# Kernel optimization log

Hardware: AMD Instinct MI355X
Metric: run time of the kernel (lower is better)

## Reference

```python
import jax, jax.numpy as jnp
import numpy as np

K_INTERACT = 8  # k nearest context nodes per target hyperedge


def setup_inputs() -> dict:
    key = jax.random.key(0)
    ks = jax.random.split(key, 7)
    B, C, H, W = 4, 256, 64, 64
    s = 1.0 / np.sqrt(C).astype(np.float32)
    return {
        "X_target": jax.random.normal(ks[0], (B, C, H, W), jnp.float32),
        "X_context1": jax.random.normal(ks[1], (B, C, H, W), jnp.float32),
        "X_context2": jax.random.normal(ks[2], (B, C, H, W), jnp.float32),
        # HypergraphConv params: node2edge Linear (W1,b1), edge2node Linear (W2,b2)
        "W1": jax.random.normal(ks[3], (C, C), jnp.float32) * s,
        "b1": jax.random.normal(ks[4], (C,), jnp.float32) * s,
        "W2": jax.random.normal(ks[5], (C, C), jnp.float32) * s,
        "b2": jax.random.normal(ks[6], (C,), jnp.float32) * s,
    }


def _hypergraph_one(Xt, Xc, W1, b1, W2, b2, k):
    """Per-batch hypergraph message passing, sparse form of H^T X / H X.
    Xt: [N, C] target nodes, Xc: [Nc, C] context nodes.
    Edge j = {target j} U {k nearest context nodes of target j}.
    Equivalent to dense H_i [N+Nc, N] with degree normalization.
    """
    N, C = Xt.shape
    Nc = Xc.shape[0]
    # squared Euclidean cdist (same argmins as torch.cdist), knn = smallest-k
    d2 = (jnp.sum(Xt * Xt, axis=1)[:, None]
          + jnp.sum(Xc * Xc, axis=1)[None, :]
          - 2.0 * (Xt @ Xc.T))                      # [N, Nc]
    _, knn = jax.lax.top_k(-d2, k)                   # [N, k] context indices

    # node2edge linear transform on all nodes
    Xn_t = Xt @ W1 + b1                              # [N, C]
    Xn_c = Xc @ W1 + b1                              # [Nc, C]

    # X_edge = (H^T @ Xn) / deg_e ; deg_e = k+1 (self + k distinct knn)
    gathered = Xn_c[knn]                             # [N, k, C]
    X_edge = (Xn_t + gathered.sum(axis=1)) / jnp.float32(k + 1)

    # edge2node linear transform
    X_et = X_edge @ W2 + b2                          # [N, C]

    # X_node_new = (H @ X_et) / deg_v
    # target node v belongs only to edge v -> deg_v = 1
    out_t = X_et
    # context node c sums X_et[j] over edges j that selected it
    flat = knn.reshape(-1)                           # [N*k]
    contrib = jax.ops.segment_sum(
        jnp.broadcast_to(X_et[:, None, :], (N, k, C)).reshape(N * k, C),
        flat, num_segments=Nc)                       # [Nc, C]
    counts = jax.ops.segment_sum(jnp.ones((N * k,), jnp.float32),
                                 flat, num_segments=Nc)
    out_c = contrib / jnp.clip(counts, 1.0)[:, None]  # deg_v clamp_min(1)
    return out_t, out_c


def reference(X_target, X_context1, X_context2, W1, b1, W2, b2):
    B, C, H, W = X_target.shape
    N = H * W
    to_nodes = lambda x: x.transpose(0, 2, 3, 1).reshape(B, N, C)
    Xt = to_nodes(X_target)                                       # [B, N, C]
    Xc = jnp.concatenate([to_nodes(X_context1), to_nodes(X_context2)],
                         axis=1)                                  # [B, 2N, C]
    f = lambda xt, xc: _hypergraph_one(xt, xc, W1, b1, W2, b2, K_INTERACT)
    out_t, out_c = jax.vmap(f)(Xt, Xc)
    to_img = lambda x: x.reshape(B, H, W, C).transpose(0, 3, 1, 2)
    return (to_img(out_t), to_img(out_c[:, :N]), to_img(out_c[:, N:]))
```

## Files before the change

### kernel.cpp

```cpp
#include <hip/hip_runtime.h>
#include <math.h>
#include <float.h>

#define BATCH 4
#define CH    256
#define NT    4096
#define NCTX  8192
#define KI    8

#define CSEL    10
#define DNSPLIT 8
#define CTX_PER (NCTX / DNSPLIT)
#define NTILE   (CTX_PER / 32)
#define NKEY    (DNSPLIT * CSEL)
#define RESC    12

typedef __attribute__((ext_vector_type(8)))  __bf16 bf16x8;
typedef __attribute__((ext_vector_type(16))) float  f32x16;

__device__ __forceinline__ unsigned short bf16_rne(float v) {
  unsigned u = __float_as_uint(v);
  return (unsigned short)((u + 0x7fffu + ((u >> 16) & 1u)) >> 16);
}

__global__ __launch_bounds__(256) void k_transpose2(const float* __restrict__ Xt,
                                                    const float* __restrict__ Xc1,
                                                    const float* __restrict__ Xc2,
                                                    float* __restrict__ Q,
                                                    float* __restrict__ P,
                                                    unsigned short* __restrict__ XtBh,
                                                    unsigned short* __restrict__ XtBl,
                                                    unsigned short* __restrict__ XcBh,
                                                    unsigned short* __restrict__ XcBl,
                                                    float* __restrict__ nrm) {
  __shared__ float tile[64][33];
  __shared__ float ps[8][32];
  const int which = blockIdx.z >> 2, b = blockIdx.z & 3;
  const float* src;
  float* dF; unsigned short *dH, *dL; float* nrmp = nullptr;
  if (which == 0) {
    src = Xt + (long)b * CH * NT;
    dF = Q + (long)b * NT * CH;
    dH = XtBh + (long)b * NT * CH;  dL = XtBl + (long)b * NT * CH;
  } else if (which == 1) {
    src = Xc1 + (long)b * CH * NT;
    dF = P + (long)b * NCTX * CH;
    dH = XcBh + (long)b * NCTX * CH;  dL = XcBl + (long)b * NCTX * CH;
    nrmp = nrm + (long)b * NCTX;
  } else {
    src = Xc2 + (long)b * CH * NT;
    dF = P + ((long)b * NCTX + NT) * CH;
    dH = XcBh + ((long)b * NCTX + NT) * CH;  dL = XcBl + ((long)b * NCTX + NT) * CH;
    nrmp = nrm + (long)b * NCTX + NT;
  }
  const int m0 = blockIdx.x * 32, c0 = blockIdx.y * 64;
  const int tx = threadIdx.x, ty = threadIdx.y;
  float part = 0.f;
#pragma unroll
  for (int i = ty; i < 64; i += 8) {
    float v = src[(long)(c0 + i) * NT + (m0 + tx)];
    tile[i][tx] = v;
    part = fmaf(v, v, part);
  }
  if (which) ps[ty][tx] = part;
  __syncthreads();
#pragma unroll
  for (int i = ty; i < 32; i += 8) {
    float v0 = tile[2 * tx][i];
    float v1 = tile[2 * tx + 1][i];
    long o = (long)(m0 + i) * CH + (c0 + 2 * tx);
    float2 f2; f2.x = v0; f2.y = v1;
    *(float2*)&dF[o] = f2;
    unsigned short h0 = bf16_rne(v0), h1 = bf16_rne(v1);
    ushort2 h2; h2.x = h0; h2.y = h1;
    *(ushort2*)&dH[o] = h2;
    float hf0 = __uint_as_float((unsigned)h0 << 16);
    float hf1 = __uint_as_float((unsigned)h1 << 16);
    ushort2 l2; l2.x = bf16_rne(v0 - hf0); l2.y = bf16_rne(v1 - hf1);
    *(ushort2*)&dL[o] = l2;
  }
  if (which && ty == 0) {
    float s = 0.f;
#pragma unroll
    for (int j = 0; j < 8; ++j) s += ps[j][tx];
    atomicAdd(&nrmp[m0 + tx], -0.5f * s);
  }
}

__global__ __launch_bounds__(256) void k_wtrans(const float* __restrict__ W1,
                                                const float* __restrict__ W2,
                                                unsigned short* __restrict__ WT1h,
                                                unsigned short* __restrict__ WT1l,
                                                unsigned short* __restrict__ WT2h,
                                                unsigned short* __restrict__ WT2l) {
  __shared__ float tile[32][33];
  const float* W = blockIdx.z ? W2 : W1;
  unsigned short* WTh = blockIdx.z ? WT2h : WT1h;
  unsigned short* WTl = blockIdx.z ? WT2l : WT1l;
  const int n0 = blockIdx.x * 32, k0 = blockIdx.y * 32;
  const int tx = threadIdx.x, ty = threadIdx.y;
#pragma unroll
  for (int i = ty; i < 32; i += 8)
    tile[i][tx] = W[(k0 + i) * CH + (n0 + tx)];
  __syncthreads();
#pragma unroll
  for (int i = ty; i < 32; i += 8) {
    float v = tile[tx][i];
    int o = (n0 + i) * CH + (k0 + tx);
    unsigned short h = bf16_rne(v);
    WTh[o] = h;
    float hf = __uint_as_float((unsigned)h << 16);
    WTl[o] = bf16_rne(v - hf);
  }
}

__global__ __launch_bounds__(256) void k_dist_mfma(const __bf16* __restrict__ XcB,
                                                   const __bf16* __restrict__ XtB,
                                                   const float* __restrict__ nrm,
                                                   unsigned* __restrict__ cand) {
  __shared__ __bf16 lds[2][32 * CH];
  const int b = blockIdx.y, split = blockIdx.z;
  const int t = threadIdx.x, w = t >> 6, lane = t & 63;
  const int l31 = lane & 31, lh = lane >> 5;
  const int tgt0 = blockIdx.x * 128 + w * 32;
  const int cbase = split * CTX_PER;
  const float* nrmt = nrm + (long)b * NCTX + cbase;

  const __bf16* tp = XtB + ((long)b * NT + tgt0 + l31) * CH + lh * 8;
  bf16x8 bfrag[16];
#pragma unroll
  for (int s = 0; s < 16; ++s) bfrag[s] = *(const bf16x8*)(tp + s * 16);

  unsigned kd[CSEL];
#pragma unroll
  for (int q = 0; q < CSEL; ++q) kd[q] = 0xFFFFFFFFu;

  const __bf16* cp = XcB + ((long)b * NCTX + cbase + l31) * CH;

  auto STAGE = [&](int buf, int jt) {
#pragma unroll
    for (int r = 0; r < 4; ++r) {
      int c = r * 4 + w;
      const __bf16* src = cp + (long)jt * 32 * CH + (c * 2 + lh) * 8;
      __bf16* dst = &lds[buf][c * 512];
      __builtin_amdgcn_global_load_lds((const __attribute__((address_space(1))) void*)src,
                                       (__attribute__((address_space(3))) void*)dst,
                                       16, 0, 0);
    }
  };

  STAGE(0, 0);
  __syncthreads();

  int cur = 0;
  for (int jt = 0; jt < NTILE; ++jt) {
    if (jt + 1 < NTILE) STAGE(cur ^ 1, jt + 1);

    const int ct0 = jt * 32;
    f32x16 acc;
#pragma unroll
    for (int g = 0; g < 4; ++g) {
      float4 nv = *(const float4*)&nrmt[ct0 + 8 * g + 4 * lh];
      acc[4 * g + 0] = nv.x; acc[4 * g + 1] = nv.y;
      acc[4 * g + 2] = nv.z; acc[4 * g + 3] = nv.w;
    }
#pragma unroll
    for (int s = 0; s < 16; ++s) {
      bf16x8 a = *(const bf16x8*)(&lds[cur][s * 512 + lane * 8]);
      acc = __builtin_amdgcn_mfma_f32_32x32x16_bf16(a, bfrag[s], acc, 0, 0, 0);
    }

#pragma unroll
    for (int reg = 0; reg < 16; ++reg) {
      const int row = (reg & 3) + 8 * (reg >> 2) + lh * 4;
      float sc = fmaf(acc[reg], -2.0f, 512.0f);
      unsigned key = (__float_as_uint(sc) & 0xFFFFF800u) | (unsigned)ct0 | (unsigned)row;
#pragma unroll
      for (int q = 0; q < CSEL; ++q) {
        unsigned lo = min(key, kd[q]);
        key = max(key, kd[q]);
        kd[q] = lo;
      }
    }
    __syncthreads();
    cur ^= 1;
  }

  unsigned oth[CSEL];
#pragma unroll
  for (int q = 0; q < CSEL; ++q) oth[q] = (unsigned)__shfl_xor((int)kd[q], 32, 64);
  if (lh == 0) {
    long ob = (((long)b * NT + tgt0 + l31) * DNSPLIT + split) * CSEL;
#pragma unroll
    for (int q = 0; q < CSEL; ++q)
      cand[ob + q] = min(kd[q], oth[CSEL - 1 - q]);
  }
}

__global__ __launch_bounds__(64) void k_rescore(const float* __restrict__ XtT,
                                                const float* __restrict__ XcT,
                                                const unsigned* __restrict__ cand,
                                                int* __restrict__ knn,
                                                unsigned* __restrict__ counts) {
  const int n = blockIdx.x, b = blockIdx.y, lane = threadIdx.x;
  const int grp = lane >> 4, gl = lane & 15;
  __shared__ unsigned sk[NKEY];
  __shared__ int cidx[RESC];
  __shared__ double sd[RESC];
  __shared__ int sj[RESC];
  const unsigned* kp = cand + ((long)b * NT + n) * NKEY;
  unsigned k0 = kp[lane];
  unsigned k1 = (lane < NKEY - 64) ? kp[64 + lane] : 0xFFFFFFFFu;
  sk[lane] = k0;
  if (lane < NKEY - 64) sk[64 + lane] = k1;
  __syncthreads();
  int r0 = 0, r1 = 0;
  for (int i = 0; i < NKEY; ++i) {
    unsigned s = sk[i];
    r0 += (s < k0 || (s == k0 && i < lane)) ? 1 : 0;
    r1 += (s < k1 || (s == k1 && i < 64 + lane)) ? 1 : 0;
  }
  if (r0 < RESC) cidx[r0] = (lane / CSEL) * CTX_PER + (int)(k0 & 0x7FFu);
  if (lane < NKEY - 64 && r1 < RESC)
    cidx[r1] = ((64 + lane) / CSEL) * CTX_PER + (int)(k1 & 0x7FFu);
  __syncthreads();

  const float* xt = XtT + ((long)b * NT + n) * CH + gl * 16;
  double xa[16];
#pragma unroll
  for (int r = 0; r < 4; ++r) {
    float4 v = *(const float4*)(xt + r * 4);
    xa[4 * r + 0] = (double)v.x; xa[4 * r + 1] = (double)v.y;
    xa[4 * r + 2] = (double)v.z; xa[4 * r + 3] = (double)v.w;
  }
#pragma unroll
  for (int q0 = 0; q0 < RESC; q0 += 4) {
    int q = q0 + grp;
    int j = cidx[q];
    const float* xc = XcT + ((long)b * NCTX + j) * CH + gl * 16;
    double acc = 0.0;
#pragma unroll
    for (int r = 0; r < 4; ++r) {
      float4 v = *(const float4*)(xc + r * 4);
      double d0 = xa[4 * r + 0] - (double)v.x; acc = fma(d0, d0, acc);
      double d1 = xa[4 * r + 1] - (double)v.y; acc = fma(d1, d1, acc);
      double d2 = xa[4 * r + 2] - (double)v.z; acc = fma(d2, d2, acc);
      double d3 = xa[4 * r + 3] - (double)v.w; acc = fma(d3, d3, acc);
    }
#pragma unroll
    for (int off = 8; off > 0; off >>= 1) acc += __shfl_xor(acc, off, 64);
    if (gl == 0) { sd[q] = acc; sj[q] = j; }
  }
  __syncthreads();
  double dq = (lane < RESC) ? sd[lane] : DBL_MAX;
  int    jq = (lane < RESC) ? sj[lane] : 0x7fffffff;
  int rank = 0;
#pragma unroll
  for (int i = 0; i < RESC; ++i) {
    double di = sd[i]; int ji = sj[i];
    rank += (di < dq || (di == dq && ji < jq)) ? 1 : 0;
  }
  if (lane < RESC && rank < KI) {
    knn[((long)b * NT + n) * KI + rank] = jq;
    atomicAdd(&counts[(long)b * NCTX + jq], 1u);
  }
}

__global__ __launch_bounds__(256) void k_gemm_mfma(const unsigned short* __restrict__ Ah,
                                                   const unsigned short* __restrict__ Al,
                                                   const unsigned short* __restrict__ WTh,
                                                   const unsigned short* __restrict__ WTl,
                                                   const float* __restrict__ bias,
                                                   float* __restrict__ out, int M) {
  __shared__ __bf16 ldsH[32 * CH];
  __shared__ __bf16 ldsL[32 * CH];
  const int b = blockIdx.y;
  const int m0 = blockIdx.x * 32;
  const int t = threadIdx.x, w = t >> 6, lane = t & 63;
  const int l31 = lane & 31, lh = lane >> 5;
  const long abase = (long)b * M * CH;
  const unsigned short* pH = Ah + abase + (long)(m0 + l31) * CH;
  const unsigned short* pL = Al + abase + (long)(m0 + l31) * CH;
#pragma unroll
  for (int r = 0; r < 4; ++r) {
    int c = r * 4 + w;
    __builtin_amdgcn_global_load_lds(
        (const __attribute__((address_space(1))) void*)(pH + (c * 2 + lh) * 8),
        (__attribute__((address_space(3))) void*)&ldsH[c * 512], 16, 0, 0);
    __builtin_amdgcn_global_load_lds(
        (const __attribute__((address_space(1))) void*)(pL + (c * 2 + lh) * 8),
        (__attribute__((address_space(3))) void*)&ldsL[c * 512], 16, 0, 0);
  }
  __syncthreads();

  const int n0 = w * 64;
  f32x16 acc0, acc1;
#pragma unroll
  for (int i = 0; i < 16; ++i) { acc0[i] = 0.f; acc1[i] = 0.f; }
#pragma unroll
  for (int s = 0; s < 16; ++s) {
    bf16x8 ah = *(const bf16x8*)&ldsH[s * 512 + lane * 8];
    bf16x8 al = *(const bf16x8*)&ldsL[s * 512 + lane * 8];
    const int koff = lh * 8 + s * 16;
    bf16x8 bh0 = *(const bf16x8*)&WTh[(n0 + l31) * CH + koff];
    bf16x8 bl0 = *(const bf16x8*)&WTl[(n0 + l31) * CH + koff];
    bf16x8 bh1 = *(const bf16x8*)&WTh[(n0 + 32 + l31) * CH + koff];
    bf16x8 bl1 = *(const bf16x8*)&WTl[(n0 + 32 + l31) * CH + koff];
    acc0 = __builtin_amdgcn_mfma_f32_32x32x16_bf16(ah, bh0, acc0, 0, 0, 0);
    acc1 = __builtin_amdgcn_mfma_f32_32x32x16_bf16(ah, bh1, acc1, 0, 0, 0);
    acc0 = __builtin_amdgcn_mfma_f32_32x32x16_bf16(ah, bl0, acc0, 0, 0, 0);
    acc1 = __builtin_amdgcn_mfma_f32_32x32x16_bf16(ah, bl1, acc1, 0, 0, 0);
    acc0 = __builtin_amdgcn_mfma_f32_32x32x16_bf16(al, bh0, acc0, 0, 0, 0);
    acc1 = __builtin_amdgcn_mfma_f32_32x32x16_bf16(al, bh1, acc1, 0, 0, 0);
  }
  float* ob = out + abase;
  float bi0 = bias[n0 + l31], bi1 = bias[n0 + 32 + l31];
#pragma unroll
  for (int reg = 0; reg < 16; ++reg) {
    int row = (reg & 3) + 8 * (reg >> 2) + 4 * lh;
    ob[(long)(m0 + row) * CH + n0 + l31]      = acc0[reg] + bi0;
    ob[(long)(m0 + row) * CH + n0 + 32 + l31] = acc1[reg] + bi1;
  }
}

__global__ __launch_bounds__(256) void k_gather(const float* __restrict__ Xn_t,
                                                const float* __restrict__ Xn_c,
                                                const int* __restrict__ knn,
                                                unsigned short* __restrict__ XeH,
                                                unsigned short* __restrict__ XeL) {
  const int n = blockIdx.x, b = blockIdx.y, c = threadIdx.x;
  const int* kn = knn + ((long)b * NT + n) * KI;
  int j[KI];
#pragma unroll
  for (int q = 0; q < KI; ++q) j[q] = kn[q];
  float acc = Xn_t[((long)b * NT + n) * CH + c];
#pragma unroll
  for (int q = 0; q < KI; ++q) acc += Xn_c[((long)b * NCTX + j[q]) * CH + c];
  float xe = acc / 9.0f;
  long o = ((long)b * NT + n) * CH + c;
  unsigned short h = bf16_rne(xe);
  XeH[o] = h;
  float hf = __uint_as_float((unsigned)h << 16);
  XeL[o] = bf16_rne(xe - hf);
}

__global__ __launch_bounds__(256) void k_scatter(const float* __restrict__ Xet,
                                                 const int* __restrict__ knn,
                                                 float* __restrict__ contrib) {
  const int n = blockIdx.x, b = blockIdx.y, c = threadIdx.x;
  const float v = Xet[((long)b * NT + n) * CH + c];
  const int* kn = knn + ((long)b * NT + n) * KI;
#pragma unroll
  for (int q = 0; q < KI; ++q)
    atomicAdd(&contrib[((long)b * NCTX + kn[q]) * CH + c], v);
}

__global__ __launch_bounds__(256) void k_fin_t(const float* __restrict__ Xet,
                                               float* __restrict__ out) {
  __shared__ float tile[32][33];
  const int b = blockIdx.z;
  const int n0 = blockIdx.x * 32, c0 = blockIdx.y * 32;
  const int tx = threadIdx.x, ty = threadIdx.y;
#pragma unroll
  for (int i = ty; i < 32; i += 8)
    tile[i][tx] = Xet[((long)b * NT + n0 + i) * CH + c0 + tx];
  __syncthreads();
#pragma unroll
  for (int i = ty; i < 32; i += 8)
    out[((long)b * CH + c0 + i) * NT + n0 + tx] = tile[tx][i];
}

__global__ __launch_bounds__(256) void k_fin_c(const float* __restrict__ contrib,
                                               const unsigned* __restrict__ counts,
                                               float* __restrict__ out1,
                                               float* __restrict__ out2) {
  __shared__ float tile[32][33];
  const int b = blockIdx.z;
  const int j0 = blockIdx.x * 32, c0 = blockIdx.y * 32;
  const int tx = threadIdx.x, ty = threadIdx.y;
#pragma unroll
  for (int i = ty; i < 32; i += 8) {
    float cnt = fmaxf((float)counts[(long)b * NCTX + j0 + i], 1.0f);
    tile[i][tx] = contrib[((long)b * NCTX + j0 + i) * CH + c0 + tx] / cnt;
  }
  __syncthreads();
  float* outp = (j0 < NT) ? (out1 + (long)b * CH * NT + j0)
                          : (out2 + (long)b * CH * NT + (j0 - NT));
#pragma unroll
  for (int i = ty; i < 32; i += 8)
    outp[(long)(c0 + i) * NT + tx] = tile[tx][i];
}

extern "C" void kernel_launch(void* const* d_in, const int* in_sizes, int n_in,
                              void* d_out, int out_size, void* d_ws, size_t ws_size,
                              hipStream_t stream) {
  const float* Xt  = (const float*)d_in[0];
  const float* Xc1 = (const float*)d_in[1];
  const float* Xc2 = (const float*)d_in[2];
  const float* W1  = (const float*)d_in[3];
  const float* b1  = (const float*)d_in[4];
  const float* W2  = (const float*)d_in[5];
  const float* b2  = (const float*)d_in[6];
  float* out = (float*)d_out;

  float* P = (float*)d_ws;
  float* Q = P + (long)BATCH * NCTX * CH;
  float* R = Q + (long)BATCH * NT * CH;
  float* nrm = R + (long)BATCH * NT * CH;
  unsigned* counts = (unsigned*)(nrm + (long)BATCH * NCTX);
  int* knn = (int*)(counts + (long)BATCH * NCTX);
  unsigned short* WT1h = (unsigned short*)(knn + (long)BATCH * NT * KI);
  unsigned short* WT1l = WT1h + CH * CH;
  unsigned short* WT2h = WT1l + CH * CH;
  unsigned short* WT2l = WT2h + CH * CH;

  unsigned* cand = (unsigned*)R;

  unsigned short* XcBh = (unsigned short*)d_out;
  unsigned short* XtBh = XcBh + (long)BATCH * NCTX * CH;
  unsigned short* XcBl = XtBh + (long)BATCH * NT * CH;
  unsigned short* XtBl = XcBl + (long)BATCH * NCTX * CH;

  float* Xn_c = P;
  float* Xn_t = R;
  unsigned short* XeH = (unsigned short*)Q;
  unsigned short* XeL = XeH + (long)BATCH * NT * CH;

  float* out_t  = out;
  float* out_c1 = out + (long)BATCH * CH * NT;
  float* out_c2 = out + 2L * BATCH * CH * NT;

  dim3 tb(32, 8);

  hipMemsetAsync(nrm, 0, (size_t)BATCH * NCTX * 8, stream);

  k_wtrans<<<dim3(8, 8, 2), tb, 0, stream>>>(W1, W2, WT1h, WT1l, WT2h, WT2l);

  k_transpose2<<<dim3(NT / 32, CH / 64, 12), tb, 0, stream>>>(
      Xt, Xc1, Xc2, Q, P, XtBh, XtBl, XcBh, XcBl, nrm);

  k_dist_mfma<<<dim3(NT / 128, BATCH, DNSPLIT), 256, 0, stream>>>(
      (const __bf16*)XcBh, (const __bf16*)XtBh, nrm, cand);

  k_rescore<<<dim3(NT, BATCH), 64, 0, stream>>>(Q, P, cand, knn, counts);

  k_gemm_mfma<<<dim3(NT / 32, BATCH), 256, 0, stream>>>(XtBh, XtBl, WT1h, WT1l, b1, Xn_t, NT);
  k_gemm_mfma<<<dim3(NCTX / 32, BATCH), 256, 0, stream>>>(XcBh, XcBl, WT1h, WT1l, b1, Xn_c, NCTX);

  k_gather<<<dim3(NT, BATCH), 256, 0, stream>>>(Xn_t, Xn_c, knn, XeH, XeL);

  k_gemm_mfma<<<dim3(NT / 32, BATCH), 256, 0, stream>>>(XeH, XeL, WT2h, WT2l, b2, R, NT);

  k_fin_t<<<dim3(NT / 32, CH / 32, BATCH), tb, 0, stream>>>(R, out_t);

  hipMemsetAsync(P, 0, (size_t)BATCH * NCTX * CH * 4, stream);
  k_scatter<<<dim3(NT, BATCH), 256, 0, stream>>>(R, knn, P);
  k_fin_c<<<dim3(NCTX / 32, CH / 32, BATCH), tb, 0, stream>>>(P, counts, out_c1, out_c2);
}
```

Baseline: 437.2 us.

## Fuse gather, edge2node GEMM and target transpose; skip top-k inserts; remap dist grid

```diff
diff --git a/kernel.cpp b/kernel.cpp
--- a/kernel.cpp
+++ b/kernel.cpp
@@ -119,10 +119,13 @@
                                                    const float* __restrict__ nrm,
                                                    unsigned* __restrict__ cand) {
   __shared__ __bf16 lds[2][32 * CH];
-  const int b = blockIdx.y, split = blockIdx.z;
+  const int lid = blockIdx.x;
+  const int xk = lid & 7, rest = lid >> 3;
+  const int b = xk >> 1, jh = xk & 1;
+  const int jw = rest & 15, split = rest >> 4;
   const int t = threadIdx.x, w = t >> 6, lane = t & 63;
   const int l31 = lane & 31, lh = lane >> 5;
-  const int tgt0 = blockIdx.x * 128 + w * 32;
+  const int tgt0 = (jh * 16 + jw) * 128 + w * 32;
   const int cbase = split * CTX_PER;
   const float* nrmt = nrm + (long)b * NCTX + cbase;
 
@@ -175,11 +178,13 @@
       const int row = (reg & 3) + 8 * (reg >> 2) + lh * 4;
       float sc = fmaf(acc[reg], -2.0f, 512.0f);
       unsigned key = (__float_as_uint(sc) & 0xFFFFF800u) | (unsigned)ct0 | (unsigned)row;
-#pragma unroll
-      for (int q = 0; q < CSEL; ++q) {
-        unsigned lo = min(key, kd[q]);
-        key = max(key, kd[q]);
-        kd[q] = lo;
+      if (__any(key < kd[CSEL - 1])) {
+#pragma unroll
+        for (int q = 0; q < CSEL; ++q) {
+          unsigned lo = min(key, kd[q]);
+          key = max(key, kd[q]);
+          kd[q] = lo;
+        }
       }
     }
     __syncthreads();
@@ -323,25 +328,116 @@
   }
 }
 
-__global__ __launch_bounds__(256) void k_gather(const float* __restrict__ Xn_t,
-                                                const float* __restrict__ Xn_c,
-                                                const int* __restrict__ knn,
-                                                unsigned short* __restrict__ XeH,
-                                                unsigned short* __restrict__ XeL) {
-  const int n = blockIdx.x, b = blockIdx.y, c = threadIdx.x;
-  const int* kn = knn + ((long)b * NT + n) * KI;
-  int j[KI];
-#pragma unroll
-  for (int q = 0; q < KI; ++q) j[q] = kn[q];
-  float acc = Xn_t[((long)b * NT + n) * CH + c];
-#pragma unroll
-  for (int q = 0; q < KI; ++q) acc += Xn_c[((long)b * NCTX + j[q]) * CH + c];
-  float xe = acc / 9.0f;
-  long o = ((long)b * NT + n) * CH + c;
-  unsigned short h = bf16_rne(xe);
-  XeH[o] = h;
-  float hf = __uint_as_float((unsigned)h << 16);
-  XeL[o] = bf16_rne(xe - hf);
+__global__ __launch_bounds__(256) void k_gg2(const float* __restrict__ Xn_c,
+                                             const int* __restrict__ knn,
+                                             const unsigned short* __restrict__ WTh,
+                                             const unsigned short* __restrict__ WTl,
+                                             const float* __restrict__ bias,
+                                             float* __restrict__ out_t,
+                                             float* __restrict__ R) {
+  __shared__ char smem[34816];
+  int* knn_s = (int*)smem;
+  __bf16* XeH = (__bf16*)(smem + 1024);
+  __bf16* XeL = (__bf16*)(smem + 17408);
+  const int b = blockIdx.y;
+  const int m0 = blockIdx.x * 32;
+  const int t = threadIdx.x, w = t >> 6, lane = t & 63;
+  const int l31 = lane & 31, lh = lane >> 5;
+
+  knn_s[t] = knn[((long)b * NT + m0 + (t >> 3)) * KI + (t & 7)];
+  __syncthreads();
+
+  const int n = t & 31, cg = t >> 5;
+  int idx[KI];
+#pragma unroll
+  for (int q = 0; q < KI; ++q) idx[q] = knn_s[n * KI + q];
+  const float* trow = R + ((long)b * NT + m0 + n) * CH;
+  const float* cb = Xn_c + (long)b * NCTX * CH;
+#pragma unroll
+  for (int kk = 0; kk < 4; ++kk) {
+    const int c = cg * 32 + kk * 8;
+    float xe[8];
+    float4 a0 = *(const float4*)(trow + c);
+    float4 a1 = *(const float4*)(trow + c + 4);
+    xe[0]=a0.x; xe[1]=a0.y; xe[2]=a0.z; xe[3]=a0.w;
+    xe[4]=a1.x; xe[5]=a1.y; xe[6]=a1.z; xe[7]=a1.w;
+#pragma unroll
+    for (int q = 0; q < KI; ++q) {
+      const float* crow = cb + (long)idx[q] * CH + c;
+      float4 c0 = *(const float4*)(crow);
+      float4 c1 = *(const float4*)(crow + 4);
+      xe[0]+=c0.x; xe[1]+=c0.y; xe[2]+=c0.z; xe[3]+=c0.w;
+      xe[4]+=c1.x; xe[5]+=c1.y; xe[6]+=c1.z; xe[7]+=c1.w;
+    }
+    unsigned h8[8], l8[8];
+#pragma unroll
+    for (int e = 0; e < 8; ++e) {
+      float v = xe[e] / 9.0f;
+      unsigned short h = bf16_rne(v);
+      h8[e] = h;
+      float hf = __uint_as_float((unsigned)h << 16);
+      l8[e] = bf16_rne(v - hf);
+    }
+    const int k8 = cg * 4 + kk;
+    const int off = (k8 >> 1) * 512 + ((k8 & 1) * 32 + n) * 8;
+    uint4 ph, pl;
+    ph.x = h8[0] | (h8[1] << 16); ph.y = h8[2] | (h8[3] << 16);
+    ph.z = h8[4] | (h8[5] << 16); ph.w = h8[6] | (h8[7] << 16);
+    pl.x = l8[0] | (l8[1] << 16); pl.y = l8[2] | (l8[3] << 16);
+    pl.z = l8[4] | (l8[5] << 16); pl.w = l8[6] | (l8[7] << 16);
+    *(uint4*)(XeH + off) = ph;
+    *(uint4*)(XeL + off) = pl;
+  }
+  __syncthreads();
+
+  const unsigned short* wh0 = WTh + (long)(w * 64 + l31) * CH;
+  const unsigned short* wl0 = WTl + (long)(w * 64 + l31) * CH;
+  f32x16 acc0, acc1;
+#pragma unroll
+  for (int i = 0; i < 16; ++i) { acc0[i] = 0.f; acc1[i] = 0.f; }
+#pragma unroll
+  for (int s = 0; s < 16; ++s) {
+    const int koff = lh * 8 + s * 16;
+    bf16x8 beh = *(const bf16x8*)&XeH[s * 512 + lane * 8];
+    bf16x8 bel = *(const bf16x8*)&XeL[s * 512 + lane * 8];
+    bf16x8 ah0 = *(const bf16x8*)(const __bf16*)(wh0 + koff);
+    bf16x8 al0 = *(const bf16x8*)(const __bf16*)(wl0 + koff);
+    bf16x8 ah1 = *(const bf16x8*)(const __bf16*)(wh0 + 32 * CH + koff);
+    bf16x8 al1 = *(const bf16x8*)(const __bf16*)(wl0 + 32 * CH + koff);
+    acc0 = __builtin_amdgcn_mfma_f32_32x32x16_bf16(ah0, beh, acc0, 0, 0, 0);
+    acc1 = __builtin_amdgcn_mfma_f32_32x32x16_bf16(ah1, beh, acc1, 0, 0, 0);
+    acc0 = __builtin_amdgcn_mfma_f32_32x32x16_bf16(al0, beh, acc0, 0, 0, 0);
+    acc1 = __builtin_amdgcn_mfma_f32_32x32x16_bf16(al1, beh, acc1, 0, 0, 0);
+    acc0 = __builtin_amdgcn_mfma_f32_32x32x16_bf16(ah0, bel, acc0, 0, 0, 0);
+    acc1 = __builtin_amdgcn_mfma_f32_32x32x16_bf16(ah1, bel, acc1, 0, 0, 0);
+  }
+  __syncthreads();
+
+  float* S = (float*)smem;
+  float* ot = out_t + (long)b * CH * NT + m0;
+#pragma unroll
+  for (int reg = 0; reg < 16; ++reg) {
+    const int row = (reg & 3) + 8 * (reg >> 2) + 4 * lh;
+    const int ch0 = w * 64 + row, ch1 = ch0 + 32;
+    float v0 = acc0[reg] + bias[ch0];
+    float v1 = acc1[reg] + bias[ch1];
+    S[ch0 * 33 + l31] = v0;
+    S[ch1 * 33 + l31] = v1;
+    ot[(long)ch0 * NT + l31] = v0;
+    ot[(long)ch1 * NT + l31] = v1;
+  }
+  __syncthreads();
+  float* rrow = R + ((long)b * NT + m0 + n) * CH;
+#pragma unroll
+  for (int kk = 0; kk < 8; ++kk) {
+    const int c = cg * 32 + kk * 4;
+    float4 v;
+    v.x = S[(c + 0) * 33 + n];
+    v.y = S[(c + 1) * 33 + n];
+    v.z = S[(c + 2) * 33 + n];
+    v.w = S[(c + 3) * 33 + n];
+    *(float4*)(rrow + c) = v;
+  }
 }
 
 __global__ __launch_bounds__(256) void k_scatter(const float* __restrict__ Xet,
@@ -353,21 +449,6 @@
 #pragma unroll
   for (int q = 0; q < KI; ++q)
     atomicAdd(&contrib[((long)b * NCTX + kn[q]) * CH + c], v);
-}
-
-__global__ __launch_bounds__(256) void k_fin_t(const float* __restrict__ Xet,
-                                               float* __restrict__ out) {
-  __shared__ float tile[32][33];
-  const int b = blockIdx.z;
-  const int n0 = blockIdx.x * 32, c0 = blockIdx.y * 32;
-  const int tx = threadIdx.x, ty = threadIdx.y;
-#pragma unroll
-  for (int i = ty; i < 32; i += 8)
-    tile[i][tx] = Xet[((long)b * NT + n0 + i) * CH + c0 + tx];
-  __syncthreads();
-#pragma unroll
-  for (int i = ty; i < 32; i += 8)
-    out[((long)b * CH + c0 + i) * NT + n0 + tx] = tile[tx][i];
 }
 
 __global__ __launch_bounds__(256) void k_fin_c(const float* __restrict__ contrib,
@@ -423,8 +504,6 @@
 
   float* Xn_c = P;
   float* Xn_t = R;
-  unsigned short* XeH = (unsigned short*)Q;
-  unsigned short* XeL = XeH + (long)BATCH * NT * CH;
 
   float* out_t  = out;
   float* out_c1 = out + (long)BATCH * CH * NT;
@@ -439,7 +518,7 @@
   k_transpose2<<<dim3(NT / 32, CH / 64, 12), tb, 0, stream>>>(
       Xt, Xc1, Xc2, Q, P, XtBh, XtBl, XcBh, XcBl, nrm);
 
-  k_dist_mfma<<<dim3(NT / 128, BATCH, DNSPLIT), 256, 0, stream>>>(
+  k_dist_mfma<<<dim3(1024), 256, 0, stream>>>(
       (const __bf16*)XcBh, (const __bf16*)XtBh, nrm, cand);
 
   k_rescore<<<dim3(NT, BATCH), 64, 0, stream>>>(Q, P, cand, knn, counts);
@@ -447,11 +526,7 @@
   k_gemm_mfma<<<dim3(NT / 32, BATCH), 256, 0, stream>>>(XtBh, XtBl, WT1h, WT1l, b1, Xn_t, NT);
   k_gemm_mfma<<<dim3(NCTX / 32, BATCH), 256, 0, stream>>>(XcBh, XcBl, WT1h, WT1l, b1, Xn_c, NCTX);
 
-  k_gather<<<dim3(NT, BATCH), 256, 0, stream>>>(Xn_t, Xn_c, knn, XeH, XeL);
-
-  k_gemm_mfma<<<dim3(NT / 32, BATCH), 256, 0, stream>>>(XeH, XeL, WT2h, WT2l, b2, R, NT);
-
-  k_fin_t<<<dim3(NT / 32, CH / 32, BATCH), tb, 0, stream>>>(R, out_t);
+  k_gg2<<<dim3(NT / 32, BATCH), 256, 0, stream>>>(Xn_c, knn, WT2h, WT2l, b2, out_t, R);
 
   hipMemsetAsync(P, 0, (size_t)BATCH * NCTX * CH * 4, stream);
   k_scatter<<<dim3(NT, BATCH), 256, 0, stream>>>(R, knn, P);
```

New measurement: 484.3 us. 1.11x slower.
